# Kernel tuning notes

Hardware: AMD Instinct MI355X
Metric: run time of the kernel (lower is better)

Reference implementation:

```python
import jax, jax.numpy as jnp
import numpy as np

N_BLOCKS = 64
BLOCK_R = 128  # rows per block (output features per block)
BLOCK_C = 128  # cols per block (input features per block)
BATCH = 4096

def setup_inputs() -> dict:
    key = jax.random.key(0)
    k1, k2 = jax.random.split(key)
    x = jax.random.normal(k1, (BATCH, N_BLOCKS * BLOCK_C), dtype=jnp.float32)
    # learned parameters: diagonal blocks, torch.randn init
    blocks = jax.random.normal(k2, (N_BLOCKS, BLOCK_R, BLOCK_C), dtype=jnp.float32)
    return {"x": x, "blocks": blocks}

def reference(x, blocks):
    # Equivalent to x @ full_matrix.T where full_matrix = blockdiag(blocks),
    # but computed directly on the blocks (no zero-fill materialization).
    B = x.shape[0]
    n, r, c = blocks.shape
    xb = x.reshape(B, n, c)                      # split input into per-block column slices
    out = jnp.einsum('bnc,nrc->bnr', xb, blocks)  # per-block GEMM: x_slice @ block.T
    return out.reshape(B, n * r)
```

## Files before the change

kernel.cpp:

```cpp
#include <hip/hip_runtime.h>
#include <hip/hip_bf16.h>


typedef __bf16 bf16_8 __attribute__((ext_vector_type(8)));
typedef __bf16 bf16_4 __attribute__((ext_vector_type(4)));
typedef float f32x4 __attribute__((ext_vector_type(4)));

#define LDS_K 136

__global__ __launch_bounds__(256, 4)
void BlocDiagLinear_kernel(const float* __restrict__ x,
                           const float* __restrict__ blocks,
                           float* __restrict__ out)
{
    __shared__ __align__(16) __bf16 ws[128 * LDS_K];

    const int bid = blockIdx.x;
    const int nb  = bid >> 5;
    const int mt  = bid & 31;

    const int t  = threadIdx.x;
    const int c4 = t & 31;
    const int r0 = t >> 5;

    const float* wg = blocks + (size_t)nb * 16384;
#pragma unroll
    for (int i = 0; i < 16; ++i) {
        const int row = i * 8 + r0;
        const float4 vw = *(const float4*)(wg + row * 128 + c4 * 4);
        bf16_4 bw = { (__bf16)vw.x, (__bf16)vw.y, (__bf16)vw.z, (__bf16)vw.w };
        *(bf16_4*)(ws + row * LDS_K + c4 * 4) = bw;
    }
    __syncthreads();

    const int lane = t & 63;
    const int w    = t >> 6;
    const int wm   = w >> 1;
    const int wn   = w & 1;
    const int lm   = lane & 15;
    const int q    = lane >> 4;

    const float* xa = x + (size_t)(mt * 128 + wm * 64 + lm) * 8192
                        + (size_t)nb * 128 + q * 8;

    f32x4 acc[4][4];
#pragma unroll
    for (int mi = 0; mi < 4; ++mi)
#pragma unroll
        for (int ni = 0; ni < 4; ++ni)
            acc[mi][ni] = (f32x4){0.f, 0.f, 0.f, 0.f};

#pragma unroll
    for (int kk = 0; kk < 4; ++kk) {
        const int k0 = kk * 32 + q * 8;
        bf16_8 a[4];
#pragma unroll
        for (int mi = 0; mi < 4; ++mi) {
            const float* p = xa + (size_t)mi * 16 * 8192 + kk * 32;
            const float4 lo = *(const float4*)(p);
            const float4 hi = *(const float4*)(p + 4);
            bf16_8 af = { (__bf16)lo.x, (__bf16)lo.y, (__bf16)lo.z, (__bf16)lo.w,
                          (__bf16)hi.x, (__bf16)hi.y, (__bf16)hi.z, (__bf16)hi.w };
            a[mi] = af;
        }
        bf16_8 b[4];
#pragma unroll
        for (int ni = 0; ni < 4; ++ni)
            b[ni] = *(const bf16_8*)(ws + (wn * 64 + ni * 16 + lm) * LDS_K + k0);
#pragma unroll
        for (int mi = 0; mi < 4; ++mi)
#pragma unroll
            for (int ni = 0; ni < 4; ++ni)
                acc[mi][ni] = __builtin_amdgcn_mfma_f32_16x16x32_bf16(
                                  a[mi], b[ni], acc[mi][ni], 0, 0, 0);
    }

    float* og = out + (size_t)(mt * 128 + wm * 64 + q * 4) * 8192
                    + (size_t)nb * 128 + wn * 64 + lm;
#pragma unroll
    for (int mi = 0; mi < 4; ++mi)
#pragma unroll
        for (int ni = 0; ni < 4; ++ni)
#pragma unroll
            for (int i = 0; i < 4; ++i)
                og[(size_t)(mi * 16 + i) * 8192 + ni * 16] = acc[mi][ni][i];
}

extern "C" void kernel_launch(void* const* d_in, const int* in_sizes, int n_in,
                              void* d_out, int out_size, void* d_ws, size_t ws_size,
                              hipStream_t stream) {
    const float* x      = (const float*)d_in[0];
    const float* blocks = (const float*)d_in[1];
    float* out          = (float*)d_out;
    BlocDiagLinear_kernel<<<dim3(64 * 32), dim3(256), 0, stream>>>(x, blocks, out);
}
```

Baseline: 263.4 us.

## Swap MFMA operand roles to vectorize output stores and pipeline x loads

The MFMA operands are swapped so the block weights from LDS become the A operand and x rows become B. Each lane then holds four consecutive output columns, so results are written as 16-byte vector stores instead of scalar strided stores. The x loads are software-pipelined one 16-row group ahead, and the block index mapping changes so consecutive workgroups share the same x rows across different diagonal blocks. Occupancy hint is lowered to 3 to make room for the extra prefetch registers, which may reduce latency hiding.

```diff
diff --git a/kernel.cpp b/kernel.cpp
--- a/kernel.cpp
+++ b/kernel.cpp
@@ -8,7 +8,7 @@
 
 #define LDS_K 136
 
-__global__ __launch_bounds__(256, 4)
+__global__ __launch_bounds__(256, 3)
 void BlocDiagLinear_kernel(const float* __restrict__ x,
                            const float* __restrict__ blocks,
                            float* __restrict__ out)
@@ -16,8 +16,8 @@
     __shared__ __align__(16) __bf16 ws[128 * LDS_K];
 
     const int bid = blockIdx.x;
-    const int nb  = bid >> 5;
-    const int mt  = bid & 31;
+    const int nb  = bid & 63;
+    const int mt  = bid >> 6;
 
     const int t  = threadIdx.x;
     const int c4 = t & 31;
@@ -40,7 +40,7 @@
     const int lm   = lane & 15;
     const int q    = lane >> 4;
 
-    const float* xa = x + (size_t)(mt * 128 + wm * 64 + lm) * 8192
+    const float* xb = x + (size_t)(mt * 128 + wn * 64 + lm) * 8192
                         + (size_t)nb * 128 + q * 8;
 
     f32x4 acc[4][4];
@@ -50,40 +50,52 @@
         for (int ni = 0; ni < 4; ++ni)
             acc[mi][ni] = (f32x4){0.f, 0.f, 0.f, 0.f};
 
+    float4 raw[8];
 #pragma unroll
     for (int kk = 0; kk < 4; ++kk) {
-        const int k0 = kk * 32 + q * 8;
-        bf16_8 a[4];
+        raw[2 * kk]     = *(const float4*)(xb + kk * 32);
+        raw[2 * kk + 1] = *(const float4*)(xb + kk * 32 + 4);
+    }
+
 #pragma unroll
-        for (int mi = 0; mi < 4; ++mi) {
-            const float* p = xa + (size_t)mi * 16 * 8192 + kk * 32;
-            const float4 lo = *(const float4*)(p);
-            const float4 hi = *(const float4*)(p + 4);
-            bf16_8 af = { (__bf16)lo.x, (__bf16)lo.y, (__bf16)lo.z, (__bf16)lo.w,
-                          (__bf16)hi.x, (__bf16)hi.y, (__bf16)hi.z, (__bf16)hi.w };
-            a[mi] = af;
-        }
+    for (int ni = 0; ni < 4; ++ni) {
         bf16_8 b[4];
 #pragma unroll
-        for (int ni = 0; ni < 4; ++ni)
-            b[ni] = *(const bf16_8*)(ws + (wn * 64 + ni * 16 + lm) * LDS_K + k0);
+        for (int kk = 0; kk < 4; ++kk) {
+            const float4 lo = raw[2 * kk];
+            const float4 hi = raw[2 * kk + 1];
+            b[kk] = (bf16_8){ (__bf16)lo.x, (__bf16)lo.y, (__bf16)lo.z, (__bf16)lo.w,
+                              (__bf16)hi.x, (__bf16)hi.y, (__bf16)hi.z, (__bf16)hi.w };
+        }
+        if (ni < 3) {
+            const float* p = xb + (size_t)(ni + 1) * 16 * 8192;
+#pragma unroll
+            for (int kk = 0; kk < 4; ++kk) {
+                raw[2 * kk]     = *(const float4*)(p + kk * 32);
+                raw[2 * kk + 1] = *(const float4*)(p + kk * 32 + 4);
+            }
+        }
+#pragma unroll
+        for (int kk = 0; kk < 4; ++kk) {
+            bf16_8 a[4];
+#pragma unroll
+            for (int mi = 0; mi < 4; ++mi)
+                a[mi] = *(const bf16_8*)(ws + (wm * 64 + mi * 16 + lm) * LDS_K
+                                            + kk * 32 + q * 8);
+#pragma unroll
+            for (int mi = 0; mi < 4; ++mi)
+                acc[mi][ni] = __builtin_amdgcn_mfma_f32_16x16x32_bf16(
+                                  a[mi], b[kk], acc[mi][ni], 0, 0, 0);
+        }
+    }
+
+    float* og = out + (size_t)(mt * 128 + wn * 64 + lm) * 8192
+                    + (size_t)nb * 128 + wm * 64 + q * 4;
+#pragma unroll
+    for (int ni = 0; ni < 4; ++ni)
 #pragma unroll
         for (int mi = 0; mi < 4; ++mi)
-#pragma unroll
-            for (int ni = 0; ni < 4; ++ni)
-                acc[mi][ni] = __builtin_amdgcn_mfma_f32_16x16x32_bf16(
-                                  a[mi], b[ni], acc[mi][ni], 0, 0, 0);
-    }
-
-    float* og = out + (size_t)(mt * 128 + wm * 64 + q * 4) * 8192
-                    + (size_t)nb * 128 + wn * 64 + lm;
-#pragma unroll
-    for (int mi = 0; mi < 4; ++mi)
-#pragma unroll
-        for (int ni = 0; ni < 4; ++ni)
-#pragma unroll
-            for (int i = 0; i < 4; ++i)
-                og[(size_t)(mi * 16 + i) * 8192 + ni * 16] = acc[mi][ni][i];
+            *(f32x4*)(og + (size_t)ni * 16 * 8192 + mi * 16) = acc[mi][ni];
 }
 
 extern "C" void kernel_launch(void* const* d_in, const int* in_sizes, int n_in,
```

Result: faster. 246.1 us (-6.5%).
